# Optimization experiments

Hardware: AMD Instinct MI355X
Metric: run time of the kernel (lower is better)

## Reference

```python
import jax, jax.numpy as jnp
import numpy as np

BN_EPS = 1e-5


def setup_inputs() -> dict:
    key = jax.random.key(0)
    ks = jax.random.split(key, 5)
    B, T, N, C, O, K, E = 2, 4, 50000, 32, 32, 3, 800000
    x = jax.random.normal(ks[0], (B, T, N, C), dtype=jnp.float32)
    edge_index = jax.random.randint(ks[1], (2, E), 0, N, dtype=jnp.int64)
    edge_weight = jax.random.uniform(ks[2], (E,), dtype=jnp.float32)
    W = jax.random.normal(ks[3], (K, C, O), dtype=jnp.float32) * 0.05
    bias = jnp.zeros((O,), dtype=jnp.float32)
    gamma = jnp.ones((O,), dtype=jnp.float32)
    beta = jnp.zeros((O,), dtype=jnp.float32)
    return {"x": x, "edge_index": edge_index, "edge_weight": edge_weight,
            "W": W, "bias": bias, "gamma": gamma, "beta": beta}


def reference(x, edge_index, edge_weight, W, bias, gamma, beta):
    # x: [B, T, N, C]; edge_index: [2, E]; W: [K, C, O]
    B, T, N, C = x.shape
    K = W.shape[0]
    src, dst = edge_index[0], edge_index[1]

    # Scaled Laplacian L_hat = 2L/lambda_max - I with sym norm, lambda_max=2
    # => L_hat = -D^{-1/2} A D^{-1/2} (zero diagonal), PyG ChebConv default.
    deg = jax.ops.segment_sum(edge_weight, src, num_segments=N)
    safe = jnp.where(deg > 0, deg, 1.0)
    dinv = jnp.where(deg > 0, 1.0 / jnp.sqrt(safe), 0.0)
    norm = -dinv[src] * edge_weight * dinv[dst]  # [E]

    # Batch all (b, t) slices together: [N, M, C] with M = B*T
    xn = jnp.transpose(x, (2, 0, 1, 3)).reshape(N, B * T, C)

    def lap(z):  # sparse SpMM applied to every (b,t) slice at once
        return jax.ops.segment_sum(norm[:, None, None] * z[src], dst,
                                   num_segments=N)

    # Chebyshev recursion: T0 = x, T1 = L_hat x, Tk = 2 L_hat T_{k-1} - T_{k-2}
    Tx_prev2 = xn
    out = jnp.einsum('nmc,co->nmo', Tx_prev2, W[0])
    if K > 1:
        Tx_prev = lap(xn)
        out = out + jnp.einsum('nmc,co->nmo', Tx_prev, W[1])
        for k in range(2, K):
            Tx_k = 2.0 * lap(Tx_prev) - Tx_prev2
            out = out + jnp.einsum('nmc,co->nmo', Tx_k, W[k])
            Tx_prev2, Tx_prev = Tx_prev, Tx_k
    out = out + bias  # [N, M, O]

    # BatchNorm1d in training mode, applied per (b,t) slice over nodes,
    # exactly as the original per-slice loop does (biased variance).
    mean = jnp.mean(out, axis=0, keepdims=True)              # [1, M, O]
    var = jnp.mean((out - mean) ** 2, axis=0, keepdims=True)  # [1, M, O]
    y = gamma * (out - mean) * jax.lax.rsqrt(var + BN_EPS) + beta
    y = jax.nn.relu(y)

    return jnp.transpose(y.reshape(N, B, T, -1), (1, 2, 0, 3))  # [B,T,N,O]
```

## Files before the change

### kernel.cpp

```cpp
#include <hip/hip_runtime.h>

#define NNODES 50000
#define NEDGES 800000
#define MB 8
#define CF 32
#define OF 32
#define FPN 256
#define TOTAL_OUT (MB * NNODES * OF)
#define NREP 8

#define BSH 9
#define BINW 512
#define NB ((NNODES + BINW - 1) / BINW)
#define NBA 512
#define EPB ((NEDGES + NBA - 1) / NBA)
#define CAPL 38
#define LBW 48
#define CH 16
#define BINCAP 14336

typedef unsigned short ushort_t;
typedef unsigned int uint_t;
typedef __attribute__((ext_vector_type(8))) short bf16x8;
typedef __attribute__((ext_vector_type(4))) float f32x4;

__device__ __forceinline__ ushort_t f2bf(float f) {
    uint_t u = __float_as_uint(f);
    u += 0x7FFFu + ((u >> 16) & 1u);
    return (ushort_t)(u >> 16);
}
__device__ __forceinline__ float bflo(uint_t u) { return __uint_as_float(u << 16); }
__device__ __forceinline__ float bfhi(uint_t u) { return __uint_as_float(u & 0xFFFF0000u); }

__device__ __forceinline__ bool detect_is64(const int* ei) {
    int lane = threadIdx.x & 63;
    int v = ei[2 * lane + 1];
    return __ballot(v != 0) == 0ULL;
}

__global__ void __launch_bounds__(256) k_build(const int* __restrict__ ei,
                                               const float* __restrict__ w,
                                               const float* __restrict__ x,
                                               float* __restrict__ deg8,
                                               int* __restrict__ g_cnt,
                                               int* __restrict__ g_real,
                                               int2* __restrict__ binD,
                                               ushort_t* __restrict__ xn) {
    int blk = blockIdx.x;
    int t = threadIdx.x;
    __shared__ int l_cnt[NB];
    __shared__ int l_base[NB];
    __shared__ int l_pfx[NB + 1];
    __shared__ int2 l_buf[NB][LBW];
    if (blk < NBA) {
        bool is64 = detect_is64(ei);
        for (int i = t; i < NB; i += 256) l_cnt[i] = 0;
        __syncthreads();
        int e0 = blk * EPB;
        int e1 = min(e0 + EPB, NEDGES);
        for (int e = e0 + t; e < e1; e += 256) {
            int s = is64 ? ei[2 * e] : ei[e];
            int d = is64 ? ei[2 * (NEDGES + e)] : ei[NEDGES + e];
            float wt = w[e];
            atomicAdd(&deg8[s * NREP + ((e >> 8) & 7)], wt);
            int bin = d >> BSH;
            int2 entry;
            entry.x = s | ((d & (BINW - 1)) << 16);
            entry.y = __float_as_int(wt);
            int pos = atomicAdd(&l_cnt[bin], 1);
            if (pos < CAPL) {
                l_buf[bin][pos] = entry;
            } else {
                int gp = atomicAdd(&g_cnt[bin], 1);
                if (gp < BINCAP) binD[(size_t)bin * BINCAP + gp] = entry;
                atomicAdd(&g_real[bin], 1);
            }
        }
        __syncthreads();
        if (t < NB) {
            int c = min(l_cnt[t], CAPL);
            int p = (c + CH - 1) & ~(CH - 1);
            for (int i = c; i < p; i++) l_buf[t][i] = make_int2(0, 0);
            l_cnt[t] = p;
            if (p > 0) l_base[t] = atomicAdd(&g_cnt[t], p);
            if (c > 0) atomicAdd(&g_real[t], c);
        }
        __syncthreads();
        if (t == 0) {
            int sacc = 0;
            for (int b2 = 0; b2 < NB; b2++) { l_pfx[b2] = sacc; sacc += l_cnt[b2]; }
            l_pfx[NB] = sacc;
        }
        __syncthreads();
        int total = l_pfx[NB];
        for (int idx = t; idx < total; idx += 256) {
            int lo = 0, hi = NB - 1;
            while (lo < hi) {
                int mid = (lo + hi + 1) >> 1;
                if (l_pfx[mid] <= idx) lo = mid; else hi = mid - 1;
            }
            int rel = idx - l_pfx[lo];
            int gp = l_base[lo] + rel;
            if (gp < BINCAP) binD[(size_t)lo * BINCAP + gp] = l_buf[lo][rel];
        }
    } else {
        int bb = blk - NBA;
        int lane = t & 63;
        int n = bb * 4 + (t >> 6);
        int m = lane >> 3;
        int c = (4 * lane) & 31;
        const float4 v = *(const float4*)(x + ((size_t)m * NNODES + n) * CF + c);
        uint2 d;
        d.x = (uint_t)f2bf(v.x) | ((uint_t)f2bf(v.y) << 16);
        d.y = (uint_t)f2bf(v.z) | ((uint_t)f2bf(v.w) << 16);
        *(uint2*)(xn + (size_t)n * FPN + 4 * lane) = d;
    }
}

__global__ void k_dinv(const float* __restrict__ deg8, float* __restrict__ dinv) {
    int n = blockIdx.x * blockDim.x + threadIdx.x;
    if (n >= NNODES) return;
    const float4* p = (const float4*)(deg8 + (size_t)n * NREP);
    float4 a = p[0], b = p[1];
    float s = a.x + a.y + a.z + a.w + b.x + b.y + b.z + b.w;
    dinv[n] = (s > 0.0f) ? (1.0f / sqrtf(s)) : 0.0f;
}

__global__ void __launch_bounds__(256) k_pass2(const int* __restrict__ g_cnt,
                                               const int* __restrict__ g_real,
                                               const int2* __restrict__ binD,
                                               int2* __restrict__ csr,
                                               int* __restrict__ csr_off) {
    __shared__ int l_ncnt[BINW];
    __shared__ int l_off[BINW];
    __shared__ int l_ws[4];
    __shared__ int l_red[4];
    int b = blockIdx.x;
    int t = threadIdx.x;
    int lane = t & 63, wv = t >> 6;

    int vb = (t < b) ? min(g_real[t], BINCAP) : 0;
    #pragma unroll
    for (int off = 32; off >= 1; off >>= 1) vb += __shfl_down(vb, off);
    if (lane == 0) l_red[wv] = vb;
    l_ncnt[t] = 0;
    l_ncnt[t + 256] = 0;
    __syncthreads();
    int base = l_red[0] + l_red[1] + l_red[2] + l_red[3];

    int cnt = min(g_cnt[b], BINCAP);
    const int2* bp = binD + (size_t)b * BINCAP;
    for (int i = t; i < cnt; i += 256) {
        int2 e = bp[i];
        if (e.y != 0) atomicAdd(&l_ncnt[e.x >> 16], 1);
    }
    __syncthreads();

    int a0 = l_ncnt[2 * t], a1 = l_ncnt[2 * t + 1];
    int psum = a0 + a1;
    int v = psum;
    #pragma unroll
    for (int off = 1; off < 64; off <<= 1) {
        int u = __shfl_up(v, off);
        if (lane >= off) v += u;
    }
    if (lane == 63) l_ws[wv] = v;
    __syncthreads();
    int wpre = 0;
    for (int i = 0; i < wv; i++) wpre += l_ws[i];
    int excl = wpre + v - psum;
    l_off[2 * t] = excl;
    l_off[2 * t + 1] = excl + a0;
    __syncthreads();

    int n0 = b * BINW;
    for (int i = t; i < BINW; i += 256) {
        int n = n0 + i;
        if (n < NNODES) csr_off[n] = base + l_off[i];
    }
    if (b == NB - 1 && t == 0)
        csr_off[NNODES] = base + l_ws[0] + l_ws[1] + l_ws[2] + l_ws[3];
    __syncthreads();

    for (int i = t; i < cnt; i += 256) {
        int2 e = bp[i];
        if (e.y != 0) {
            int dl = e.x >> 16;
            int slot = atomicAdd(&l_off[dl], 1);
            csr[(size_t)base + slot] = make_int2(e.x & 0xFFFF, e.y);
        }
    }
}

template <int PHASE>
__global__ void __launch_bounds__(256) k_spmm(const ushort_t* __restrict__ src,
                                              const ushort_t* __restrict__ xn0,
                                              const int* __restrict__ csr_off,
                                              const int2* __restrict__ csr,
                                              const float* __restrict__ dinv,
                                              ushort_t* __restrict__ dst) {
    int t = threadIdx.x;
    int lane = t & 63;
    int n = __builtin_amdgcn_readfirstlane(blockIdx.x * 4 + (t >> 6));
    int off = csr_off[n];
    int cnt = min(csr_off[n + 1] - off, 64);
    float dn = dinv[n];
    float a0 = 0.0f, a1 = 0.0f, a2 = 0.0f, a3 = 0.0f;
    if (cnt > 0) {
        int j = off + min(lane, cnt - 1);
        int2 ed = csr[j];
        int cv = ed.x;
        float vw = -dinv[cv] * __int_as_float(ed.y) * dn;
        uint_t vv = __float_as_uint(vw);
        for (int k = 0; k < cnt; k += 16) {
            int sc[16]; float v[16];
            #pragma unroll
            for (int i = 0; i < 16; i++) {
                sc[i] = __builtin_amdgcn_readlane(cv, k + i);
                float vr = __uint_as_float(__builtin_amdgcn_readlane((int)vv, k + i));
                v[i] = (k + i < cnt) ? vr : 0.0f;
            }
            uint2 u[16];
            #pragma unroll
            for (int i = 0; i < 16; i++)
                u[i] = *(const uint2*)(src + (size_t)sc[i] * FPN + 4 * lane);
            #pragma unroll
            for (int i = 0; i < 16; i++) {
                a0 += v[i] * bflo(u[i].x);
                a1 += v[i] * bfhi(u[i].x);
                a2 += v[i] * bflo(u[i].y);
                a3 += v[i] * bfhi(u[i].y);
            }
        }
    }
    if (PHASE == 2) {
        const uint2 xu = *(const uint2*)(xn0 + (size_t)n * FPN + 4 * lane);
        a0 = 2.0f * a0 - bflo(xu.x);
        a1 = 2.0f * a1 - bfhi(xu.x);
        a2 = 2.0f * a2 - bflo(xu.y);
        a3 = 2.0f * a3 - bfhi(xu.y);
    }
    uint2 d;
    d.x = (uint_t)f2bf(a0) | ((uint_t)f2bf(a1) << 16);
    d.y = (uint_t)f2bf(a2) | ((uint_t)f2bf(a3) << 16);
    *(uint2*)(dst + (size_t)n * FPN + 4 * lane) = d;
}

__global__ void k_wprep(const float* __restrict__ W, ushort_t* __restrict__ wbf) {
    int tid = threadIdx.x;
    for (int i = tid; i < 384; i += 256) {
        int k    = i >> 7;
        int rem  = i & 127;
        int oh   = rem >> 6;
        int lane = rem & 63;
        int quad = lane >> 4;
        int colc = lane & 15;
        ushort_t* d = wbf + (size_t)i * 8;
        for (int j = 0; j < 8; j++) {
            int c = quad * 8 + j;
            int o = oh * 16 + colc;
            d[j] = f2bf(W[k * (CF * OF) + c * OF + o]);
        }
    }
}

__global__ void __launch_bounds__(256) k_wfuse(const ushort_t* __restrict__ xn,
                                               const ushort_t* __restrict__ t1,
                                               const ushort_t* __restrict__ t2,
                                               const ushort_t* __restrict__ wbf,
                                               const float* __restrict__ bias,
                                               float* __restrict__ out) {
    int t = threadIdx.x;
    int lane = t & 63;
    int wv = blockIdx.x * 4 + (t >> 6);
    if (wv >= NNODES / 16) return;
    int n0 = wv * 16;
    int quad = lane >> 4, col = lane & 15;

    bf16x8 B[6];
    #pragma unroll
    for (int i = 0; i < 6; i++)
        B[i] = *(const bf16x8*)(wbf + (size_t)(i * 64 + lane) * 8);
    float blo = bias[col], bhi = bias[16 + col];

    size_t aoff = (size_t)(n0 + col) * FPN + quad * 8;
    #pragma unroll
    for (int m = 0; m < 8; m++) {
        bf16x8 A0 = *(const bf16x8*)(xn + aoff + m * 32);
        bf16x8 A1 = *(const bf16x8*)(t1 + aoff + m * 32);
        bf16x8 A2 = *(const bf16x8*)(t2 + aoff + m * 32);
        f32x4 lo = { blo, blo, blo, blo };
        f32x4 hi = { bhi, bhi, bhi, bhi };
        lo = __builtin_amdgcn_mfma_f32_16x16x32_bf16(A0, B[0], lo, 0, 0, 0);
        hi = __builtin_amdgcn_mfma_f32_16x16x32_bf16(A0, B[1], hi, 0, 0, 0);
        lo = __builtin_amdgcn_mfma_f32_16x16x32_bf16(A1, B[2], lo, 0, 0, 0);
        hi = __builtin_amdgcn_mfma_f32_16x16x32_bf16(A1, B[3], hi, 0, 0, 0);
        lo = __builtin_amdgcn_mfma_f32_16x16x32_bf16(A2, B[4], lo, 0, 0, 0);
        hi = __builtin_amdgcn_mfma_f32_16x16x32_bf16(A2, B[5], hi, 0, 0, 0);
        float* ob = out + ((size_t)m * NNODES + n0 + quad * 4) * OF + col;
        #pragma unroll
        for (int r = 0; r < 4; r++) {
            ob[(size_t)r * OF]      = lo[r];
            ob[(size_t)r * OF + 16] = hi[r];
        }
    }
}

__global__ void __launch_bounds__(256) k_stats(const float* __restrict__ out,
                                               float* __restrict__ stats) {
    int m = blockIdx.y;
    int t = threadIdx.x;
    int o4 = t & 7, row = t >> 3;
    int n0 = blockIdx.x * 1024;
    int nend = min(n0 + 1024, NNODES);
    float sx = 0, sy = 0, sz = 0, sw = 0;
    float qx = 0, qy = 0, qz = 0, qw = 0;
    for (int n = n0 + row; n < nend; n += 32) {
        const float4 v = *(const float4*)(out + ((size_t)m * NNODES + n) * OF + o4 * 4);
        sx += v.x; sy += v.y; sz += v.z; sw += v.w;
        qx += v.x * v.x; qy += v.y * v.y; qz += v.z * v.z; qw += v.w * v.w;
    }
    __shared__ float4 sS[256];
    __shared__ float4 sQ[256];
    sS[t] = make_float4(sx, sy, sz, sw);
    sQ[t] = make_float4(qx, qy, qz, qw);
    __syncthreads();
    for (int off = 16; off >= 1; off >>= 1) {
        if (row < off) {
            float4 a = sS[t], b = sS[t + off * 8];
            sS[t] = make_float4(a.x + b.x, a.y + b.y, a.z + b.z, a.w + b.w);
            float4 c = sQ[t], d = sQ[t + off * 8];
            sQ[t] = make_float4(c.x + d.x, c.y + d.y, c.z + d.z, c.w + d.w);
        }
        __syncthreads();
    }
    if (row == 0) {
        float4 s = sS[t], q = sQ[t];
        int base = m * 32 + o4 * 4;
        atomicAdd(&stats[base + 0], s.x);
        atomicAdd(&stats[base + 1], s.y);
        atomicAdd(&stats[base + 2], s.z);
        atomicAdd(&stats[base + 3], s.w);
        atomicAdd(&stats[256 + base + 0], q.x);
        atomicAdd(&stats[256 + base + 1], q.y);
        atomicAdd(&stats[256 + base + 2], q.z);
        atomicAdd(&stats[256 + base + 3], q.w);
    }
}

__global__ void __launch_bounds__(256) k_final(float* __restrict__ out,
                                               const float* __restrict__ stats,
                                               const float* __restrict__ gamma,
                                               const float* __restrict__ beta) {
    int idx4 = blockIdx.x * 256 + threadIdx.x;
    size_t base = (size_t)idx4 * 4;
    int o = (int)(base & 31);
    int m = (int)(base / ((size_t)NNODES * OF));
    int mo = m * 32 + o;
    const float4 sm = *(const float4*)(stats + mo);
    const float4 sq = *(const float4*)(stats + 256 + mo);
    const float4 g  = *(const float4*)(gamma + o);
    const float4 bt = *(const float4*)(beta + o);
    const float inv_n = 1.0f / (float)NNODES;
    float4 v = *(const float4*)(out + base);
    {
        float mean = sm.x * inv_n, var = sq.x * inv_n - mean * mean;
        float sc = g.x * rsqrtf(var + 1e-5f);
        v.x = fmaxf(v.x * sc + (bt.x - sc * mean), 0.0f);
    }
    {
        float mean = sm.y * inv_n, var = sq.y * inv_n - mean * mean;
        float sc = g.y * rsqrtf(var + 1e-5f);
        v.y = fmaxf(v.y * sc + (bt.y - sc * mean), 0.0f);
    }
    {
        float mean = sm.z * inv_n, var = sq.z * inv_n - mean * mean;
        float sc = g.z * rsqrtf(var + 1e-5f);
        v.z = fmaxf(v.z * sc + (bt.z - sc * mean), 0.0f);
    }
    {
        float mean = sm.w * inv_n, var = sq.w * inv_n - mean * mean;
        float sc = g.w * rsqrtf(var + 1e-5f);
        v.w = fmaxf(v.w * sc + (bt.w - sc * mean), 0.0f);
    }
    *(float4*)(out + base) = v;
}

extern "C" void kernel_launch(void* const* d_in, const int* in_sizes, int n_in,
                              void* d_out, int out_size, void* d_ws, size_t ws_size,
                              hipStream_t stream) {
    const float* x     = (const float*)d_in[0];
    const int*   ei    = (const int*)d_in[1];
    const float* w     = (const float*)d_in[2];
    const float* W     = (const float*)d_in[3];
    const float* bias  = (const float*)d_in[4];
    const float* gamma = (const float*)d_in[5];
    const float* beta  = (const float*)d_in[6];
    float* out = (float*)d_out;

    char* p = (char*)d_ws;
    auto alloc = [&](size_t bytes) {
        char* r = p;
        p += (bytes + 511) & ~(size_t)511;
        return r;
    };
    int*      g_cnt   = (int*)alloc((size_t)NB * 4);
    int*      g_real  = (int*)alloc((size_t)NB * 4);
    float*    stats   = (float*)alloc(512 * 4);
    float*    deg8    = (float*)alloc((size_t)NNODES * NREP * 4);
    float*    dinv    = (float*)alloc((size_t)NNODES * 4);
    int2*     binD    = (int2*)alloc((size_t)NB * BINCAP * 8);
    int2*     csr     = (int2*)alloc((size_t)NEDGES * 8);
    int*      csr_off = (int*)alloc((size_t)(NNODES + 1) * 4);
    ushort_t* wbf     = (ushort_t*)alloc(384 * 8 * 2);
    ushort_t* xn      = (ushort_t*)alloc((size_t)NNODES * FPN * 2);
    ushort_t* t1      = (ushort_t*)alloc((size_t)NNODES * FPN * 2);
    ushort_t* t2      = (ushort_t*)alloc((size_t)NNODES * FPN * 2);

    size_t zlen = (char*)(deg8 + (size_t)NNODES * NREP) - (char*)g_cnt;
    hipMemsetAsync(g_cnt, 0, zlen, stream);

    k_wprep<<<1, 256, 0, stream>>>(W, wbf);
    k_build<<<NBA + NNODES / 4, 256, 0, stream>>>(ei, w, x, deg8, g_cnt, g_real,
                                                  binD, xn);
    k_dinv<<<(NNODES + 255) / 256, 256, 0, stream>>>(deg8, dinv);
    k_pass2<<<NB, 256, 0, stream>>>(g_cnt, g_real, binD, csr, csr_off);

    k_spmm<1><<<NNODES / 4, 256, 0, stream>>>(xn, xn, csr_off, csr, dinv, t1);
    k_spmm<2><<<NNODES / 4, 256, 0, stream>>>(t1, xn, csr_off, csr, dinv, t2);

    int wfblocks = (NNODES / 16 + 3) / 4;
    k_wfuse<<<wfblocks, 256, 0, stream>>>(xn, t1, t2, wbf, bias, out);

    dim3 sgrid((NNODES + 1023) / 1024, MB);
    k_stats<<<sgrid, 256, 0, stream>>>(out, stats);
    k_final<<<TOTAL_OUT / 4 / 256, 256, 0, stream>>>(out, stats, gamma, beta);
}
```

Baseline: 373.9 us.

## Fuse BN statistics into MFMA output kernel and merge dinv into pass2

The output GEMM kernel now accumulates per-block sum and sum-of-squares into shared memory and writes per-block partials, which a small reduction kernel sums. This replaces the separate stats kernel that re-read the whole output. The dinv computation moves into extra blocks of k_pass2, removing one launch. The edge-index loads now use int2 vector reads, and the local bin buffer capacity shrinks, which lowers LDS use but sends more entries to global overflow. The new reduction runs serially over about 782 partials per thread in only 2 blocks, and the shared-memory atomics add contention.

```diff
diff --git a/kernel.cpp b/kernel.cpp
--- a/kernel.cpp
+++ b/kernel.cpp
@@ -14,10 +14,12 @@
 #define NB ((NNODES + BINW - 1) / BINW)
 #define NBA 512
 #define EPB ((NEDGES + NBA - 1) / NBA)
-#define CAPL 38
-#define LBW 48
+#define CAPL 30
+#define LBW 32
 #define CH 16
 #define BINCAP 14336
+#define WFB ((NNODES / 16 + 3) / 4)
+#define DGRID ((NNODES + 1023) / 1024)
 
 typedef unsigned short ushort_t;
 typedef unsigned int uint_t;
@@ -54,13 +56,20 @@
     __shared__ int2 l_buf[NB][LBW];
     if (blk < NBA) {
         bool is64 = detect_is64(ei);
+        const int2* ei2 = (const int2*)ei;
         for (int i = t; i < NB; i += 256) l_cnt[i] = 0;
         __syncthreads();
         int e0 = blk * EPB;
         int e1 = min(e0 + EPB, NEDGES);
         for (int e = e0 + t; e < e1; e += 256) {
-            int s = is64 ? ei[2 * e] : ei[e];
-            int d = is64 ? ei[2 * (NEDGES + e)] : ei[NEDGES + e];
+            int s, d;
+            if (is64) {
+                int2 sv = ei2[e];
+                int2 dv = ei2[NEDGES + e];
+                s = sv.x; d = dv.x;
+            } else {
+                s = ei[e]; d = ei[NEDGES + e];
+            }
             float wt = w[e];
             atomicAdd(&deg8[s * NREP + ((e >> 8) & 7)], wt);
             int bin = d >> BSH;
@@ -117,26 +126,32 @@
     }
 }
 
-__global__ void k_dinv(const float* __restrict__ deg8, float* __restrict__ dinv) {
-    int n = blockIdx.x * blockDim.x + threadIdx.x;
-    if (n >= NNODES) return;
-    const float4* p = (const float4*)(deg8 + (size_t)n * NREP);
-    float4 a = p[0], b = p[1];
-    float s = a.x + a.y + a.z + a.w + b.x + b.y + b.z + b.w;
-    dinv[n] = (s > 0.0f) ? (1.0f / sqrtf(s)) : 0.0f;
-}
-
 __global__ void __launch_bounds__(256) k_pass2(const int* __restrict__ g_cnt,
                                                const int* __restrict__ g_real,
                                                const int2* __restrict__ binD,
+                                               const float* __restrict__ deg8,
                                                int2* __restrict__ csr,
-                                               int* __restrict__ csr_off) {
+                                               int* __restrict__ csr_off,
+                                               float* __restrict__ dinv) {
     __shared__ int l_ncnt[BINW];
     __shared__ int l_off[BINW];
     __shared__ int l_ws[4];
     __shared__ int l_red[4];
     int b = blockIdx.x;
     int t = threadIdx.x;
+    if (b >= NB) {
+        int n = (b - NB) * 1024 + t;
+        #pragma unroll
+        for (int i = 0; i < 4; i++, n += 256) {
+            if (n < NNODES) {
+                const float4* p4 = (const float4*)(deg8 + (size_t)n * NREP);
+                float4 a = p4[0], b4 = p4[1];
+                float s = a.x + a.y + a.z + a.w + b4.x + b4.y + b4.z + b4.w;
+                dinv[n] = (s > 0.0f) ? (1.0f / sqrtf(s)) : 0.0f;
+            }
+        }
+        return;
+    }
     int lane = t & 63, wv = t >> 6;
 
     int vb = (t < b) ? min(g_real[t], BINCAP) : 0;
@@ -269,12 +284,18 @@
                                                const ushort_t* __restrict__ t2,
                                                const ushort_t* __restrict__ wbf,
                                                const float* __restrict__ bias,
-                                               float* __restrict__ out) {
+                                               float* __restrict__ out,
+                                               float* __restrict__ pstats) {
+    __shared__ float ls[256];
+    __shared__ float lq[256];
     int t = threadIdx.x;
+    ls[t] = 0.0f;
+    lq[t] = 0.0f;
+    __syncthreads();
     int lane = t & 63;
-    int wv = blockIdx.x * 4 + (t >> 6);
-    if (wv >= NNODES / 16) return;
-    int n0 = wv * 16;
+    int wv4 = blockIdx.x * 4 + (t >> 6);
+    bool valid = (wv4 < NNODES / 16);
+    int n0 = wv4 * 16;
     int quad = lane >> 4, col = lane & 15;
 
     bf16x8 B[6];
@@ -286,66 +307,45 @@
     size_t aoff = (size_t)(n0 + col) * FPN + quad * 8;
     #pragma unroll
     for (int m = 0; m < 8; m++) {
-        bf16x8 A0 = *(const bf16x8*)(xn + aoff + m * 32);
-        bf16x8 A1 = *(const bf16x8*)(t1 + aoff + m * 32);
-        bf16x8 A2 = *(const bf16x8*)(t2 + aoff + m * 32);
-        f32x4 lo = { blo, blo, blo, blo };
-        f32x4 hi = { bhi, bhi, bhi, bhi };
-        lo = __builtin_amdgcn_mfma_f32_16x16x32_bf16(A0, B[0], lo, 0, 0, 0);
-        hi = __builtin_amdgcn_mfma_f32_16x16x32_bf16(A0, B[1], hi, 0, 0, 0);
-        lo = __builtin_amdgcn_mfma_f32_16x16x32_bf16(A1, B[2], lo, 0, 0, 0);
-        hi = __builtin_amdgcn_mfma_f32_16x16x32_bf16(A1, B[3], hi, 0, 0, 0);
-        lo = __builtin_amdgcn_mfma_f32_16x16x32_bf16(A2, B[4], lo, 0, 0, 0);
-        hi = __builtin_amdgcn_mfma_f32_16x16x32_bf16(A2, B[5], hi, 0, 0, 0);
-        float* ob = out + ((size_t)m * NNODES + n0 + quad * 4) * OF + col;
-        #pragma unroll
-        for (int r = 0; r < 4; r++) {
-            ob[(size_t)r * OF]      = lo[r];
-            ob[(size_t)r * OF + 16] = hi[r];
-        }
-    }
-}
-
-__global__ void __launch_bounds__(256) k_stats(const float* __restrict__ out,
-                                               float* __restrict__ stats) {
-    int m = blockIdx.y;
-    int t = threadIdx.x;
-    int o4 = t & 7, row = t >> 3;
-    int n0 = blockIdx.x * 1024;
-    int nend = min(n0 + 1024, NNODES);
-    float sx = 0, sy = 0, sz = 0, sw = 0;
-    float qx = 0, qy = 0, qz = 0, qw = 0;
-    for (int n = n0 + row; n < nend; n += 32) {
-        const float4 v = *(const float4*)(out + ((size_t)m * NNODES + n) * OF + o4 * 4);
-        sx += v.x; sy += v.y; sz += v.z; sw += v.w;
-        qx += v.x * v.x; qy += v.y * v.y; qz += v.z * v.z; qw += v.w * v.w;
-    }
-    __shared__ float4 sS[256];
-    __shared__ float4 sQ[256];
-    sS[t] = make_float4(sx, sy, sz, sw);
-    sQ[t] = make_float4(qx, qy, qz, qw);
-    __syncthreads();
-    for (int off = 16; off >= 1; off >>= 1) {
-        if (row < off) {
-            float4 a = sS[t], b = sS[t + off * 8];
-            sS[t] = make_float4(a.x + b.x, a.y + b.y, a.z + b.z, a.w + b.w);
-            float4 c = sQ[t], d = sQ[t + off * 8];
-            sQ[t] = make_float4(c.x + d.x, c.y + d.y, c.z + d.z, c.w + d.w);
-        }
-        __syncthreads();
-    }
-    if (row == 0) {
-        float4 s = sS[t], q = sQ[t];
-        int base = m * 32 + o4 * 4;
-        atomicAdd(&stats[base + 0], s.x);
-        atomicAdd(&stats[base + 1], s.y);
-        atomicAdd(&stats[base + 2], s.z);
-        atomicAdd(&stats[base + 3], s.w);
-        atomicAdd(&stats[256 + base + 0], q.x);
-        atomicAdd(&stats[256 + base + 1], q.y);
-        atomicAdd(&stats[256 + base + 2], q.z);
-        atomicAdd(&stats[256 + base + 3], q.w);
-    }
+        if (valid) {
+            bf16x8 A0 = *(const bf16x8*)(xn + aoff + m * 32);
+            bf16x8 A1 = *(const bf16x8*)(t1 + aoff + m * 32);
+            bf16x8 A2 = *(const bf16x8*)(t2 + aoff + m * 32);
+            f32x4 lo = { blo, blo, blo, blo };
+            f32x4 hi = { bhi, bhi, bhi, bhi };
+            lo = __builtin_amdgcn_mfma_f32_16x16x32_bf16(A0, B[0], lo, 0, 0, 0);
+            hi = __builtin_amdgcn_mfma_f32_16x16x32_bf16(A0, B[1], hi, 0, 0, 0);
+            lo = __builtin_amdgcn_mfma_f32_16x16x32_bf16(A1, B[2], lo, 0, 0, 0);
+            hi = __builtin_amdgcn_mfma_f32_16x16x32_bf16(A1, B[3], hi, 0, 0, 0);
+            lo = __builtin_amdgcn_mfma_f32_16x16x32_bf16(A2, B[4], lo, 0, 0, 0);
+            hi = __builtin_amdgcn_mfma_f32_16x16x32_bf16(A2, B[5], hi, 0, 0, 0);
+            float* ob = out + ((size_t)m * NNODES + n0 + quad * 4) * OF + col;
+            #pragma unroll
+            for (int r = 0; r < 4; r++) {
+                ob[(size_t)r * OF]      = lo[r];
+                ob[(size_t)r * OF + 16] = hi[r];
+            }
+            float s0 = lo[0] + lo[1] + lo[2] + lo[3];
+            float q0 = lo[0]*lo[0] + lo[1]*lo[1] + lo[2]*lo[2] + lo[3]*lo[3];
+            float s1 = hi[0] + hi[1] + hi[2] + hi[3];
+            float q1 = hi[0]*hi[0] + hi[1]*hi[1] + hi[2]*hi[2] + hi[3]*hi[3];
+            atomicAdd(&ls[m * 32 + col], s0);
+            atomicAdd(&lq[m * 32 + col], q0);
+            atomicAdd(&ls[m * 32 + 16 + col], s1);
+            atomicAdd(&lq[m * 32 + 16 + col], q1);
+        }
+    }
+    __syncthreads();
+    pstats[(size_t)blockIdx.x * 512 + t]       = ls[t];
+    pstats[(size_t)blockIdx.x * 512 + 256 + t] = lq[t];
+}
+
+__global__ void __launch_bounds__(256) k_red(const float* __restrict__ pstats,
+                                             float* __restrict__ stats) {
+    int i = blockIdx.x * 256 + threadIdx.x;
+    float s = 0.0f;
+    for (int b = 0; b < WFB; b++) s += pstats[(size_t)b * 512 + i];
+    stats[i] = s;
 }
 
 __global__ void __launch_bounds__(256) k_final(float* __restrict__ out,
@@ -406,12 +406,13 @@
     };
     int*      g_cnt   = (int*)alloc((size_t)NB * 4);
     int*      g_real  = (int*)alloc((size_t)NB * 4);
+    float*    deg8    = (float*)alloc((size_t)NNODES * NREP * 4);
     float*    stats   = (float*)alloc(512 * 4);
-    float*    deg8    = (float*)alloc((size_t)NNODES * NREP * 4);
     float*    dinv    = (float*)alloc((size_t)NNODES * 4);
     int2*     binD    = (int2*)alloc((size_t)NB * BINCAP * 8);
     int2*     csr     = (int2*)alloc((size_t)NEDGES * 8);
     int*      csr_off = (int*)alloc((size_t)(NNODES + 1) * 4);
+    float*    pstats  = (float*)alloc((size_t)WFB * 512 * 4);
     ushort_t* wbf     = (ushort_t*)alloc(384 * 8 * 2);
     ushort_t* xn      = (ushort_t*)alloc((size_t)NNODES * FPN * 2);
     ushort_t* t1      = (ushort_t*)alloc((size_t)NNODES * FPN * 2);
@@ -423,16 +424,13 @@
     k_wprep<<<1, 256, 0, stream>>>(W, wbf);
     k_build<<<NBA + NNODES / 4, 256, 0, stream>>>(ei, w, x, deg8, g_cnt, g_real,
                                                   binD, xn);
-    k_dinv<<<(NNODES + 255) / 256, 256, 0, stream>>>(deg8, dinv);
-    k_pass2<<<NB, 256, 0, stream>>>(g_cnt, g_real, binD, csr, csr_off);
+    k_pass2<<<NB + DGRID, 256, 0, stream>>>(g_cnt, g_real, binD, deg8,
+                                            csr, csr_off, dinv);
 
     k_spmm<1><<<NNODES / 4, 256, 0, stream>>>(xn, xn, csr_off, csr, dinv, t1);
     k_spmm<2><<<NNODES / 4, 256, 0, stream>>>(t1, xn, csr_off, csr, dinv, t2);
 
-    int wfblocks = (NNODES / 16 + 3) / 4;
-    k_wfuse<<<wfblocks, 256, 0, stream>>>(xn, t1, t2, wbf, bias, out);
-
-    dim3 sgrid((NNODES + 1023) / 1024, MB);
-    k_stats<<<sgrid, 256, 0, stream>>>(out, stats);
+    k_wfuse<<<WFB, 256, 0, stream>>>(xn, t1, t2, wbf, bias, out, pstats);
+    k_red<<<2, 256, 0, stream>>>(pstats, stats);
     k_final<<<TOTAL_OUT / 4 / 256, 256, 0, stream>>>(out, stats, gamma, beta);
 }
```

Measured after the change: 395.0 us. 1.06x slower.

## Split CSR build into half-bins, stage CSR in LDS, fuse dinv into pass2

Applied to the files above, without the earlier changes.

Each destination bin is split into two 256-node halves, so pass2 runs on twice as many blocks. Each block sorts its edges into an LDS staging buffer and then writes the CSR with coalesced stores instead of scattered global writes. The degree replicas move to a per-block, node-contiguous layout, and the dinv computation becomes extra blocks inside pass2, which removes one kernel launch. Edge indices are read as int2, and the local bin buffer shrinks to raise occupancy in k_build. Each half-bin block still scans the whole bin, and the LDS staging is capped, so an oversized half-bin would silently drop edges.

```diff
diff --git a/kernel.cpp b/kernel.cpp
--- a/kernel.cpp
+++ b/kernel.cpp
@@ -12,12 +12,16 @@
 #define BSH 9
 #define BINW 512
 #define NB ((NNODES + BINW - 1) / BINW)
+#define PH (NB * 2)
 #define NBA 512
 #define EPB ((NEDGES + NBA - 1) / NBA)
-#define CAPL 38
-#define LBW 48
+#define CAPL 30
+#define LBW 32
 #define CH 16
 #define BINCAP 14336
+#define STCAP 7168
+#define WFB ((NNODES / 16 + 3) / 4)
+#define DGRID ((NNODES + 1023) / 1024)
 
 typedef unsigned short ushort_t;
 typedef unsigned int uint_t;
@@ -43,37 +47,51 @@
                                                const float* __restrict__ x,
                                                float* __restrict__ deg8,
                                                int* __restrict__ g_cnt,
-                                               int* __restrict__ g_real,
+                                               int* __restrict__ g_realH,
                                                int2* __restrict__ binD,
                                                ushort_t* __restrict__ xn) {
     int blk = blockIdx.x;
     int t = threadIdx.x;
     __shared__ int l_cnt[NB];
     __shared__ int l_base[NB];
-    __shared__ int l_pfx[NB + 1];
+    __shared__ ushort_t l_pfx[NB + 1];
+    __shared__ int l_half[PH];
     __shared__ int2 l_buf[NB][LBW];
     if (blk < NBA) {
         bool is64 = detect_is64(ei);
+        const int2* ei2 = (const int2*)ei;
         for (int i = t; i < NB; i += 256) l_cnt[i] = 0;
+        for (int i = t; i < PH; i += 256) l_half[i] = 0;
         __syncthreads();
+        int rep = blk & 7;
         int e0 = blk * EPB;
         int e1 = min(e0 + EPB, NEDGES);
         for (int e = e0 + t; e < e1; e += 256) {
-            int s = is64 ? ei[2 * e] : ei[e];
-            int d = is64 ? ei[2 * (NEDGES + e)] : ei[NEDGES + e];
+            int s, d;
+            if (is64) {
+                int2 sv = ei2[e];
+                int2 dv = ei2[NEDGES + e];
+                s = sv.x; d = dv.x;
+            } else {
+                s = ei[e]; d = ei[NEDGES + e];
+            }
             float wt = w[e];
-            atomicAdd(&deg8[s * NREP + ((e >> 8) & 7)], wt);
+            atomicAdd(&deg8[(size_t)rep * NNODES + s], wt);
             int bin = d >> BSH;
+            int half = (d >> 8) & 1;
             int2 entry;
             entry.x = s | ((d & (BINW - 1)) << 16);
             entry.y = __float_as_int(wt);
             int pos = atomicAdd(&l_cnt[bin], 1);
             if (pos < CAPL) {
                 l_buf[bin][pos] = entry;
+                atomicAdd(&l_half[bin * 2 + half], 1);
             } else {
                 int gp = atomicAdd(&g_cnt[bin], 1);
-                if (gp < BINCAP) binD[(size_t)bin * BINCAP + gp] = entry;
-                atomicAdd(&g_real[bin], 1);
+                if (gp < BINCAP) {
+                    binD[(size_t)bin * BINCAP + gp] = entry;
+                    atomicAdd(&g_realH[bin * 2 + half], 1);
+                }
             }
         }
         __syncthreads();
@@ -83,13 +101,17 @@
             for (int i = c; i < p; i++) l_buf[t][i] = make_int2(0, 0);
             l_cnt[t] = p;
             if (p > 0) l_base[t] = atomicAdd(&g_cnt[t], p);
-            if (c > 0) atomicAdd(&g_real[t], c);
-        }
+        }
+        for (int i = t; i < PH; i += 256)
+            if (l_half[i] > 0) atomicAdd(&g_realH[i], l_half[i]);
         __syncthreads();
         if (t == 0) {
             int sacc = 0;
-            for (int b2 = 0; b2 < NB; b2++) { l_pfx[b2] = sacc; sacc += l_cnt[b2]; }
-            l_pfx[NB] = sacc;
+            for (int b2 = 0; b2 < NB; b2++) {
+                l_pfx[b2] = (ushort_t)sacc;
+                sacc += l_cnt[b2];
+            }
+            l_pfx[NB] = (ushort_t)sacc;
         }
         __syncthreads();
         int total = l_pfx[NB];
@@ -97,9 +119,9 @@
             int lo = 0, hi = NB - 1;
             while (lo < hi) {
                 int mid = (lo + hi + 1) >> 1;
-                if (l_pfx[mid] <= idx) lo = mid; else hi = mid - 1;
-            }
-            int rel = idx - l_pfx[lo];
+                if ((int)l_pfx[mid] <= idx) lo = mid; else hi = mid - 1;
+            }
+            int rel = idx - (int)l_pfx[lo];
             int gp = l_base[lo] + rel;
             if (gp < BINCAP) binD[(size_t)lo * BINCAP + gp] = l_buf[lo][rel];
         }
@@ -117,48 +139,55 @@
     }
 }
 
-__global__ void k_dinv(const float* __restrict__ deg8, float* __restrict__ dinv) {
-    int n = blockIdx.x * blockDim.x + threadIdx.x;
-    if (n >= NNODES) return;
-    const float4* p = (const float4*)(deg8 + (size_t)n * NREP);
-    float4 a = p[0], b = p[1];
-    float s = a.x + a.y + a.z + a.w + b.x + b.y + b.z + b.w;
-    dinv[n] = (s > 0.0f) ? (1.0f / sqrtf(s)) : 0.0f;
-}
-
 __global__ void __launch_bounds__(256) k_pass2(const int* __restrict__ g_cnt,
-                                               const int* __restrict__ g_real,
+                                               const int* __restrict__ g_realH,
                                                const int2* __restrict__ binD,
+                                               const float* __restrict__ deg8,
                                                int2* __restrict__ csr,
-                                               int* __restrict__ csr_off) {
-    __shared__ int l_ncnt[BINW];
-    __shared__ int l_off[BINW];
+                                               int* __restrict__ csr_off,
+                                               float* __restrict__ dinv) {
+    __shared__ int2 l_stage[STCAP];
+    __shared__ int l_h[256];
     __shared__ int l_ws[4];
     __shared__ int l_red[4];
+    __shared__ int l_tot;
     int b = blockIdx.x;
     int t = threadIdx.x;
+    if (b >= PH) {
+        int n = (b - PH) * 1024 + t;
+        #pragma unroll
+        for (int i = 0; i < 4; i++, n += 256) {
+            if (n < NNODES) {
+                float s = 0.0f;
+                #pragma unroll
+                for (int r = 0; r < NREP; r++) s += deg8[(size_t)r * NNODES + n];
+                dinv[n] = (s > 0.0f) ? (1.0f / sqrtf(s)) : 0.0f;
+            }
+        }
+        return;
+    }
+    int bin = b >> 1, h = b & 1;
     int lane = t & 63, wv = t >> 6;
 
-    int vb = (t < b) ? min(g_real[t], BINCAP) : 0;
+    int vb = (t < b) ? g_realH[t] : 0;
     #pragma unroll
     for (int off = 32; off >= 1; off >>= 1) vb += __shfl_down(vb, off);
     if (lane == 0) l_red[wv] = vb;
-    l_ncnt[t] = 0;
-    l_ncnt[t + 256] = 0;
+    l_h[t] = 0;
     __syncthreads();
     int base = l_red[0] + l_red[1] + l_red[2] + l_red[3];
 
-    int cnt = min(g_cnt[b], BINCAP);
-    const int2* bp = binD + (size_t)b * BINCAP;
+    int cnt = min(g_cnt[bin], BINCAP);
+    const int2* bp = binD + (size_t)bin * BINCAP;
     for (int i = t; i < cnt; i += 256) {
         int2 e = bp[i];
-        if (e.y != 0) atomicAdd(&l_ncnt[e.x >> 16], 1);
-    }
-    __syncthreads();
-
-    int a0 = l_ncnt[2 * t], a1 = l_ncnt[2 * t + 1];
-    int psum = a0 + a1;
-    int v = psum;
+        int dl = e.x >> 16;
+        if (e.y != 0 && (dl >> 8) == h) atomicAdd(&l_h[dl & 255], 1);
+    }
+    __syncthreads();
+
+    int a0 = l_h[t];
+    int v = a0;
     #pragma unroll
     for (int off = 1; off < 64; off <<= 1) {
         int u = __shfl_up(v, off);
@@ -168,28 +197,29 @@
     __syncthreads();
     int wpre = 0;
     for (int i = 0; i < wv; i++) wpre += l_ws[i];
-    int excl = wpre + v - psum;
-    l_off[2 * t] = excl;
-    l_off[2 * t + 1] = excl + a0;
-    __syncthreads();
-
-    int n0 = b * BINW;
-    for (int i = t; i < BINW; i += 256) {
-        int n = n0 + i;
-        if (n < NNODES) csr_off[n] = base + l_off[i];
-    }
-    if (b == NB - 1 && t == 0)
-        csr_off[NNODES] = base + l_ws[0] + l_ws[1] + l_ws[2] + l_ws[3];
+    int excl = wpre + v - a0;
+
+    int n = bin * BINW + h * 256 + t;
+    if (n < NNODES) csr_off[n] = base + excl;
+    l_h[t] = excl;
+    if (t == 255) {
+        l_tot = excl + a0;
+        if (b == PH - 1) csr_off[NNODES] = base + excl + a0;
+    }
     __syncthreads();
 
     for (int i = t; i < cnt; i += 256) {
         int2 e = bp[i];
-        if (e.y != 0) {
-            int dl = e.x >> 16;
-            int slot = atomicAdd(&l_off[dl], 1);
-            csr[(size_t)base + slot] = make_int2(e.x & 0xFFFF, e.y);
-        }
-    }
+        int dl = e.x >> 16;
+        if (e.y != 0 && (dl >> 8) == h) {
+            int slot = atomicAdd(&l_h[dl & 255], 1);
+            if (slot < STCAP) l_stage[slot] = make_int2(e.x & 0xFFFF, e.y);
+        }
+    }
+    __syncthreads();
+
+    int tot = min(l_tot, STCAP);
+    for (int i = t; i < tot; i += 256) csr[(size_t)base + i] = l_stage[i];
 }
 
 template <int PHASE>
@@ -405,7 +435,7 @@
         return r;
     };
     int*      g_cnt   = (int*)alloc((size_t)NB * 4);
-    int*      g_real  = (int*)alloc((size_t)NB * 4);
+    int*      g_realH = (int*)alloc((size_t)PH * 4);
     float*    stats   = (float*)alloc(512 * 4);
     float*    deg8    = (float*)alloc((size_t)NNODES * NREP * 4);
     float*    dinv    = (float*)alloc((size_t)NNODES * 4);
@@ -421,16 +451,15 @@
     hipMemsetAsync(g_cnt, 0, zlen, stream);
 
     k_wprep<<<1, 256, 0, stream>>>(W, wbf);
-    k_build<<<NBA + NNODES / 4, 256, 0, stream>>>(ei, w, x, deg8, g_cnt, g_real,
+    k_build<<<NBA + NNODES / 4, 256, 0, stream>>>(ei, w, x, deg8, g_cnt, g_realH,
                                                   binD, xn);
-    k_dinv<<<(NNODES + 255) / 256, 256, 0, stream>>>(deg8, dinv);
-    k_pass2<<<NB, 256, 0, stream>>>(g_cnt, g_real, binD, csr, csr_off);
+    k_pass2<<<PH + DGRID, 256, 0, stream>>>(g_cnt, g_realH, binD, deg8,
+                                            csr, csr_off, dinv);
 
     k_spmm<1><<<NNODES / 4, 256, 0, stream>>>(xn, xn, csr_off, csr, dinv, t1);
     k_spmm<2><<<NNODES / 4, 256, 0, stream>>>(t1, xn, csr_off, csr, dinv, t2);
 
-    int wfblocks = (NNODES / 16 + 3) / 4;
-    k_wfuse<<<wfblocks, 256, 0, stream>>>(xn, t1, t2, wbf, bias, out);
+    k_wfuse<<<WFB, 256, 0, stream>>>(xn, t1, t2, wbf, bias, out);
 
     dim3 sgrid((NNODES + 1023) / 1024, MB);
     k_stats<<<sgrid, 256, 0, stream>>>(out, stats);
```

After: 357.9 us. 1.04x faster.
